# Optimization experiments

Hardware: AMD Instinct MI355X
Metric: run time of the kernel (lower is better)

The kernel has to match this reference:

```python
import jax, jax.numpy as jnp
import numpy as np

D_MODEL = 1024
N_HEADS = 16


def setup_inputs() -> dict:
    key = jax.random.key(0)
    ks = jax.random.split(key, 16)
    B, L, S, D = 4, 2048, 2048, D_MODEL
    inp = {
        "q": jax.random.normal(ks[0], (B, L, D), jnp.float32),
        "k": jax.random.normal(ks[1], (B, S, D), jnp.float32),
        "v": jax.random.normal(ks[2], (B, S, D), jnp.float32),
        "tau": jax.random.uniform(ks[3], (B, 1), jnp.float32, 0.5, 1.5),
        "delta": jax.random.normal(ks[4], (B, S), jnp.float32),
    }
    s = 1.0 / np.sqrt(D)
    inp["Wq"] = jax.random.normal(ks[5], (D, D), jnp.float32) * s
    inp["bq"] = jnp.zeros((D,), jnp.float32)
    inp["Wk"] = jax.random.normal(ks[6], (D, D), jnp.float32) * s
    inp["bk"] = jnp.zeros((D,), jnp.float32)
    inp["Wv"] = jax.random.normal(ks[7], (D, D), jnp.float32) * s
    inp["bv"] = jnp.zeros((D,), jnp.float32)
    inp["Wo"] = jax.random.normal(ks[8], (D, D), jnp.float32) * s
    inp["bo"] = jnp.zeros((D,), jnp.float32)
    return inp


def reference(q, k, v, tau, delta, Wq, bq, Wk, bk, Wv, bv, Wo, bo):
    B, L, D = q.shape
    S = k.shape[1]
    H = N_HEADS
    E = D // H
    # Linear projections (torch Linear: x @ W.T + b), split heads
    qh = (q @ Wq.T + bq).reshape(B, L, H, E)
    kh = (k @ Wk.T + bk).reshape(B, S, H, E)
    vh = (v @ Wv.T + bv).reshape(B, S, H, E)
    scale = 1.0 / np.sqrt(E).astype(np.float32)
    # de-stationary attention: scores * tau + delta, then scaled softmax
    scores = jnp.einsum('blhe,bshe->bhls', qh, kh)
    scores = scores * tau[:, None, None, :] + delta[:, None, None, :]
    a = jax.nn.softmax(scale * scores, axis=-1)  # dropout: eval mode (identity)
    out = jnp.einsum('bhls,bshd->blhd', a, vh).reshape(B, L, D)
    return out @ Wo.T + bo
```

## Files before the change

### kernel.cpp

```cpp
#include <hip/hip_runtime.h>
#include <hip/hip_bf16.h>
#include <stdint.h>

typedef unsigned short u16;
typedef __attribute__((ext_vector_type(8))) short short8;
typedef __attribute__((ext_vector_type(4))) short short4v;
typedef __attribute__((ext_vector_type(4))) float f32x4;
typedef __attribute__((ext_vector_type(16))) float f32x16;
typedef __attribute__((ext_vector_type(2))) unsigned int uint2v;
typedef __attribute__((ext_vector_type(4))) unsigned int uint4v;

#define DEV static __device__ __forceinline__

DEV u16 f2bf(float f) {
  union { float f; unsigned u; } x; x.f = f;
  unsigned r = x.u + 0x7FFFu + ((x.u >> 16) & 1u);
  return (u16)(r >> 16);
}

DEV unsigned cvtpk_bf16(float a, float b) {
  unsigned r;
  asm("v_cvt_pk_bf16_f32 %0, %1, %2" : "=v"(r) : "v"(a), "v"(b));
  return r;
}

DEV void pl32swap(unsigned& a, unsigned& b) {
  asm("v_permlane32_swap_b32 %0, %1" : "+v"(a), "+v"(b));
}

DEV void gld_lds16(const void* g, void* l) {
  __builtin_amdgcn_global_load_lds(
      (const __attribute__((address_space(1))) unsigned int*)(g),
      (__attribute__((address_space(3))) unsigned int*)(l),
      16, 0, 0);
}

DEV f32x16 zero16() {
  f32x16 z = {0.f,0.f,0.f,0.f,0.f,0.f,0.f,0.f,0.f,0.f,0.f,0.f,0.f,0.f,0.f,0.f};
  return z;
}

__global__ void cvt3(const float* __restrict__ a, const float* __restrict__ b,
                     const float* __restrict__ c, u16* __restrict__ oa,
                     u16* __restrict__ ob, u16* __restrict__ oc, int n4) {
  int i = blockIdx.x * blockDim.x + threadIdx.x;
  if (i >= n4) return;
  const float* in = (blockIdx.y == 0) ? a : (blockIdx.y == 1) ? b : c;
  u16* out = (blockIdx.y == 0) ? oa : (blockIdx.y == 1) ? ob : oc;
  float4 v = ((const float4*)in)[i];
  short4v o;
  o[0] = (short)f2bf(v.x); o[1] = (short)f2bf(v.y);
  o[2] = (short)f2bf(v.z); o[3] = (short)f2bf(v.w);
  ((short4v*)out)[i] = o;
}

__global__ void cvt4(const float* __restrict__ a, const float* __restrict__ b,
                     const float* __restrict__ c, const float* __restrict__ d,
                     u16* __restrict__ oa, u16* __restrict__ ob,
                     u16* __restrict__ oc, u16* __restrict__ od, int n4) {
  int i = blockIdx.x * blockDim.x + threadIdx.x;
  if (i >= n4) return;
  const float* in = (blockIdx.y == 0) ? a : (blockIdx.y == 1) ? b : (blockIdx.y == 2) ? c : d;
  u16* out = (blockIdx.y == 0) ? oa : (blockIdx.y == 1) ? ob : (blockIdx.y == 2) ? oc : od;
  float4 v = ((const float4*)in)[i];
  short4v o;
  o[0] = (short)f2bf(v.x); o[1] = (short)f2bf(v.y);
  o[2] = (short)f2bf(v.z); o[3] = (short)f2bf(v.w);
  ((short4v*)out)[i] = o;
}

__global__ void scale_delta(const float* __restrict__ in, float* __restrict__ out, int n4) {
  int i = blockIdx.x * blockDim.x + threadIdx.x;
  if (i >= n4) return;
  constexpr float C = 0.125f * 1.44269504f;
  float4 v = ((const float4*)in)[i];
  f32x4 o = {v.x * C, v.y * C, v.z * C, v.w * C};
  ((f32x4*)out)[i] = o;
}

template<int OMODE>
__global__ __launch_bounds__(256, 2)
void gemm_nt(const u16* __restrict__ A, const u16* __restrict__ Bt,
             const float* __restrict__ bias, void* __restrict__ out) {
  constexpr int Mn = 8192, Nn = 1024, Kn = 1024;
  constexpr int BM = 128, BN = 128, BK = 64;
  __shared__ __align__(16) u16 As[BM * BK];
  __shared__ __align__(16) u16 Bs[BN * BK];
  constexpr int nbn = Nn / BN;
  constexpr int nwg = (Mn / BM) * nbn;
  int bid = blockIdx.x;
  int swz = (bid & 7) * (nwg >> 3) + (bid >> 3);
  int bm = (swz / nbn) * BM;
  int bn = (swz % nbn) * BN;
  int tid = threadIdx.x;
  int lane = tid & 63, w = tid >> 6;
  int l15 = lane & 15, l4 = lane >> 4;
  int wm = (w >> 1) * 64, wn = (w & 1) * 64;
  int swl = (w << 6);

  f32x4 acc[4][4];
#pragma unroll
  for (int i = 0; i < 4; ++i)
#pragma unroll
    for (int j = 0; j < 4; ++j) acc[i][j] = (f32x4){0.f, 0.f, 0.f, 0.f};

  const u16* Ag = A + (size_t)bm * Kn;
  const u16* Bg = Bt + (size_t)bn * Kn;

  for (int kt = 0; kt < Kn / BK; ++kt) {
    int k0 = kt * BK;
#pragma unroll
    for (int j = 0; j < 4; ++j) {
      int flat = j * 256 + tid;
      int row = flat >> 3, u = flat & 7;
      int gu = u ^ (row & 7);
      gld_lds16(Ag + (size_t)row * Kn + k0 + gu * 8, &As[(j * 256 + swl) * 8]);
    }
#pragma unroll
    for (int j = 0; j < 4; ++j) {
      int flat = j * 256 + tid;
      int row = flat >> 3, u = flat & 7;
      int gu = u ^ (row & 7);
      gld_lds16(Bg + (size_t)row * Kn + k0 + gu * 8, &Bs[(j * 256 + swl) * 8]);
    }
    __syncthreads();
#pragma unroll
    for (int ks = 0; ks < 2; ++ks) {
      short8 af[4], bfr[4];
#pragma unroll
      for (int i = 0; i < 4; ++i) {
        int ra = wm + i * 16 + l15;
        int ua = (ks * 4 + l4) ^ (ra & 7);
        af[i] = *(const short8*)&As[ra * 64 + ua * 8];
        int rb = wn + i * 16 + l15;
        int ub = (ks * 4 + l4) ^ (rb & 7);
        bfr[i] = *(const short8*)&Bs[rb * 64 + ub * 8];
      }
#pragma unroll
      for (int mi = 0; mi < 4; ++mi)
#pragma unroll
        for (int ni = 0; ni < 4; ++ni)
          acc[mi][ni] = __builtin_amdgcn_mfma_f32_16x16x32_bf16(af[mi], bfr[ni], acc[mi][ni], 0, 0, 0);
    }
    __syncthreads();
  }

#pragma unroll
  for (int ni = 0; ni < 4; ++ni) {
    int n = bn + wn + ni * 16 + l15;
    float bv = bias[n];
    int h = n >> 6, e = n & 63;
#pragma unroll
    for (int mi = 0; mi < 4; ++mi) {
      int m0 = bm + wm + mi * 16 + l4 * 4;
      if (OMODE == 2) {
        float* o = (float*)out;
#pragma unroll
        for (int j = 0; j < 4; ++j)
          o[(size_t)(m0 + j) * Nn + n] = acc[mi][ni][j] + bv;
      } else if (OMODE == 0) {
        u16* o = (u16*)out;
#pragma unroll
        for (int j = 0; j < 4; ++j) {
          int m = m0 + j;
          int b = m >> 11, l = m & 2047;
          int idx = ((b * 16 + h) * 2048 + l) * 64 + e;
          o[idx] = f2bf(acc[mi][ni][j] + bv);
        }
      } else {
        u16* o = (u16*)out;
        int b = m0 >> 11, s = m0 & 2047;
        short4v pk;
#pragma unroll
        for (int j = 0; j < 4; ++j) pk[j] = (short)f2bf(acc[mi][ni][j] + bv);
        int idx = ((b * 16 + h) * 64 + e) * 2048 + s;
        *(short4v*)&o[idx] = pk;
      }
    }
  }
}

DEV float softpack(const f32x16 sc, float st2, const float* dlp, int hi,
                   short8& f0, short8& f1) {
  float pe[16];
#pragma unroll
  for (int g = 0; g < 4; ++g) {
    f32x4 dlv = *(const f32x4*)(dlp + g * 8 + hi * 4);
#pragma unroll
    for (int m = 0; m < 4; ++m)
      pe[g * 4 + m] = __builtin_amdgcn_exp2f(sc[g * 4 + m] * st2 + dlv[m]);
  }
  float ps = 0.f;
#pragma unroll
  for (int i = 0; i < 16; i += 4) ps += (pe[i] + pe[i + 1]) + (pe[i + 2] + pe[i + 3]);
  unsigned a0 = cvtpk_bf16(pe[0], pe[1]), a1 = cvtpk_bf16(pe[2], pe[3]);
  unsigned b0 = cvtpk_bf16(pe[4], pe[5]), b1 = cvtpk_bf16(pe[6], pe[7]);
  pl32swap(a0, b0);
  pl32swap(a1, b1);
  f0 = __builtin_bit_cast(short8, (uint4v){a0, a1, b0, b1});
  unsigned c0 = cvtpk_bf16(pe[8], pe[9]), c1 = cvtpk_bf16(pe[10], pe[11]);
  unsigned d0 = cvtpk_bf16(pe[12], pe[13]), d1 = cvtpk_bf16(pe[14], pe[15]);
  pl32swap(c0, d0);
  pl32swap(c1, d1);
  f1 = __builtin_bit_cast(short8, (uint4v){c0, c1, d0, d1});
  return ps;
}

__global__ __launch_bounds__(512, 4)
void flash_attn(const u16* __restrict__ qh, const u16* __restrict__ kh,
                const u16* __restrict__ vt, const float* __restrict__ tau,
                const float* __restrict__ dl2g, u16* __restrict__ attn) {
  constexpr int S = 2048, E = 64;
  __shared__ __align__(16) u16 Ks[2][64 * 64];
  __shared__ __align__(16) u16 Vs[2][64 * 64];
  __shared__ __align__(16) float dls[2][64];

  int bh = blockIdx.x & 63, qb = blockIdx.x >> 6;
  int b = bh >> 4, h = bh & 15;
  int tid = threadIdx.x, lane = tid & 63, w = tid >> 6;
  int l31 = lane & 31, hi = lane >> 5;
  int q0 = qb * 256 + w * 32;

  int srow = tid >> 3, sgu = (tid & 7) ^ ((tid >> 3) & 7);

  const u16* Qg = qh + ((size_t)bh * S + q0) * E;
  short8 qf[4];
#pragma unroll
  for (int ec = 0; ec < 4; ++ec)
    qf[ec] = *(const short8*)&Qg[l31 * E + ec * 16 + hi * 8];

  float st2 = tau[b] * (0.125f * 1.44269504f);
  float l_run = 0.f;
  f32x16 oa0 = zero16(), oa1 = zero16();

  const u16* Kg = kh + (size_t)bh * S * E;
  const u16* Vg = vt + (size_t)bh * E * S;
  const float* Dg = dl2g + (size_t)b * S;

  gld_lds16(Kg + (size_t)srow * E + sgu * 8, &Ks[0][w * 512]);
  gld_lds16(Vg + (size_t)srow * S + sgu * 8, &Vs[0][w * 512]);
  if (tid < 16) gld_lds16(Dg + tid * 4, &dls[0][0]);
  __syncthreads();

  for (int t = 0; t < S / 64; ++t) {
    int cur = t & 1, nxt = cur ^ 1;
    if (t < S / 64 - 1) {
      int s1 = (t + 1) * 64;
      gld_lds16(Kg + (size_t)(s1 + srow) * E + sgu * 8, &Ks[nxt][w * 512]);
      gld_lds16(Vg + (size_t)srow * S + s1 + sgu * 8, &Vs[nxt][w * 512]);
      if (tid < 16) gld_lds16(Dg + s1 + tid * 4, &dls[nxt][0]);
    }

    const char* KsB = (const char*)&Ks[cur][0];
    f32x16 sc0 = zero16(), sc1 = zero16();
    __builtin_amdgcn_s_setprio(1);
#pragma unroll
    for (int ec = 0; ec < 4; ++ec) {
      int uo = (((ec * 2 + hi) ^ (l31 & 7)) * 16) + l31 * 128;
      short8 kf0 = *(const short8*)(KsB + uo);
      short8 kf1 = *(const short8*)(KsB + 4096 + uo);
      sc0 = __builtin_amdgcn_mfma_f32_32x32x16_bf16(kf0, qf[ec], sc0, 0, 0, 0);
      sc1 = __builtin_amdgcn_mfma_f32_32x32x16_bf16(kf1, qf[ec], sc1, 0, 0, 0);
    }
    __builtin_amdgcn_s_setprio(0);

    short8 pf0, pf1, pf2, pf3;
    float psum = softpack(sc0, st2, &dls[cur][0], hi, pf0, pf1);
    psum += softpack(sc1, st2, &dls[cur][32], hi, pf2, pf3);
    psum += __shfl_xor(psum, 32);
    l_run += psum;

    const char* VsB = (const char*)&Vs[cur][0];
    __builtin_amdgcn_s_setprio(1);
#pragma unroll
    for (int ksb = 0; ksb < 4; ++ksb) {
      int uo = (((ksb * 2 + hi) ^ (l31 & 7)) * 16) + l31 * 128;
      short8 v0 = *(const short8*)(VsB + uo);
      short8 v1 = *(const short8*)(VsB + 4096 + uo);
      short8 pf = (ksb == 0) ? pf0 : (ksb == 1) ? pf1 : (ksb == 2) ? pf2 : pf3;
      oa0 = __builtin_amdgcn_mfma_f32_32x32x16_bf16(v0, pf, oa0, 0, 0, 0);
      oa1 = __builtin_amdgcn_mfma_f32_32x32x16_bf16(v1, pf, oa1, 0, 0, 0);
    }
    __builtin_amdgcn_s_setprio(0);
    __syncthreads();
  }

  float li = 1.f / l_run;
  u16* Og = attn + ((((size_t)b * 2048 + q0 + l31) * 16 + h) * 64);
#pragma unroll
  for (int g = 0; g < 4; ++g) {
    uint2v s0, s1;
    s0[0] = cvtpk_bf16(oa0[g * 4 + 0] * li, oa0[g * 4 + 1] * li);
    s0[1] = cvtpk_bf16(oa0[g * 4 + 2] * li, oa0[g * 4 + 3] * li);
    *(uint2v*)&Og[g * 8 + hi * 4] = s0;
    s1[0] = cvtpk_bf16(oa1[g * 4 + 0] * li, oa1[g * 4 + 1] * li);
    s1[1] = cvtpk_bf16(oa1[g * 4 + 2] * li, oa1[g * 4 + 3] * li);
    *(uint2v*)&Og[32 + g * 8 + hi * 4] = s1;
  }
}

extern "C" void kernel_launch(void* const* d_in, const int* in_sizes, int n_in,
                              void* d_out, int out_size, void* d_ws, size_t ws_size,
                              hipStream_t stream) {
  const float* q = (const float*)d_in[0];
  const float* k = (const float*)d_in[1];
  const float* v = (const float*)d_in[2];
  const float* tau = (const float*)d_in[3];
  const float* delta = (const float*)d_in[4];
  const float* Wq = (const float*)d_in[5];
  const float* bq = (const float*)d_in[6];
  const float* Wk = (const float*)d_in[7];
  const float* bk = (const float*)d_in[8];
  const float* Wv = (const float*)d_in[9];
  const float* bv = (const float*)d_in[10];
  const float* Wo = (const float*)d_in[11];
  const float* bo = (const float*)d_in[12];

  const size_t SZ_ACT = (size_t)8192 * 1024 * 2;
  const size_t SZ_W = (size_t)1024 * 1024 * 2;
  char* p = (char*)d_ws;
  u16* qbf = (u16*)p; p += SZ_ACT;
  u16* kbf = (u16*)p; p += SZ_ACT;
  u16* vbf = (u16*)p; p += SZ_ACT;
  u16* wq = (u16*)p; p += SZ_W;
  u16* wk = (u16*)p; p += SZ_W;
  u16* wv = (u16*)p; p += SZ_W;
  u16* wo = (u16*)p; p += SZ_W;
  float* dl2g = (float*)p; p += 8192 * 4;
  u16* qhb = (u16*)p; p += SZ_ACT;
  u16* khb = (u16*)p; p += SZ_ACT;
  u16* vtb = (u16*)p; p += SZ_ACT;
  u16* attn = qbf;

  cvt3<<<dim3(8192, 3), 256, 0, stream>>>(q, k, v, qbf, kbf, vbf, 2097152);
  cvt4<<<dim3(1024, 4), 256, 0, stream>>>(Wq, Wk, Wv, Wo, wq, wk, wv, wo, 262144);
  scale_delta<<<8, 256, 0, stream>>>(delta, dl2g, 2048);

  gemm_nt<0><<<512, 256, 0, stream>>>(qbf, wq, bq, qhb);
  gemm_nt<0><<<512, 256, 0, stream>>>(kbf, wk, bk, khb);
  gemm_nt<1><<<512, 256, 0, stream>>>(vbf, wv, bv, vtb);
  flash_attn<<<512, 512, 0, stream>>>(qhb, khb, vtb, tau, dl2g, attn);
  gemm_nt<2><<<512, 256, 0, stream>>>(attn, wo, bo, d_out);
}
```

Baseline: 213.1 us.

## Batch QKV projections into one launch and shrink attention blocks to four waves

The three Q/K/V projection GEMMs become a single 1536-block launch that picks weights, bias and output layout per block, which relies on the contiguous workspace layout of the converted activations and weights. Flash attention now uses 256-thread blocks covering 128 queries, giving 1024 blocks for better occupancy and tail balance. Its K/V LDS staging switches from XOR-swizzled rows to a column-chunk layout with simpler address math. The new LDS layout changes the bank-conflict behaviour, and each block now loads K/V tiles for half as many queries, doubling total K/V traffic.

```diff
diff --git a/kernel.cpp b/kernel.cpp
--- a/kernel.cpp
+++ b/kernel.cpp
@@ -78,16 +78,115 @@
   ((f32x4*)out)[i] = o;
 }
 
-template<int OMODE>
 __global__ __launch_bounds__(256, 2)
-void gemm_nt(const u16* __restrict__ A, const u16* __restrict__ Bt,
-             const float* __restrict__ bias, void* __restrict__ out) {
-  constexpr int Mn = 8192, Nn = 1024, Kn = 1024;
+void gemm_qkv(const u16* __restrict__ A, const u16* __restrict__ W,
+              const float* __restrict__ bq, const float* __restrict__ bk,
+              const float* __restrict__ bv, u16* __restrict__ qhb,
+              u16* __restrict__ khb, u16* __restrict__ vtb) {
+  constexpr int Nn = 1024, Kn = 1024;
   constexpr int BM = 128, BN = 128, BK = 64;
   __shared__ __align__(16) u16 As[BM * BK];
   __shared__ __align__(16) u16 Bs[BN * BK];
   constexpr int nbn = Nn / BN;
-  constexpr int nwg = (Mn / BM) * nbn;
+  constexpr int nwg = (24576 / BM) * nbn;
+  int bid = blockIdx.x;
+  int swz = (bid & 7) * (nwg >> 3) + (bid >> 3);
+  int bm = (swz / nbn) * BM;
+  int bn = (swz % nbn) * BN;
+  int mat = bm >> 13;
+  int bml = bm & 8191;
+  int tid = threadIdx.x;
+  int lane = tid & 63, w = tid >> 6;
+  int l15 = lane & 15, l4 = lane >> 4;
+  int wm = (w >> 1) * 64, wn = (w & 1) * 64;
+  int swl = (w << 6);
+
+  f32x4 acc[4][4];
+#pragma unroll
+  for (int i = 0; i < 4; ++i)
+#pragma unroll
+    for (int j = 0; j < 4; ++j) acc[i][j] = (f32x4){0.f, 0.f, 0.f, 0.f};
+
+  const u16* Ag = A + (size_t)bm * Kn;
+  const u16* Bg = W + ((size_t)mat << 20) + (size_t)bn * Kn;
+
+  for (int kt = 0; kt < Kn / BK; ++kt) {
+    int k0 = kt * BK;
+#pragma unroll
+    for (int j = 0; j < 4; ++j) {
+      int flat = j * 256 + tid;
+      int row = flat >> 3, u = flat & 7;
+      int gu = u ^ (row & 7);
+      gld_lds16(Ag + (size_t)row * Kn + k0 + gu * 8, &As[(j * 256 + swl) * 8]);
+    }
+#pragma unroll
+    for (int j = 0; j < 4; ++j) {
+      int flat = j * 256 + tid;
+      int row = flat >> 3, u = flat & 7;
+      int gu = u ^ (row & 7);
+      gld_lds16(Bg + (size_t)row * Kn + k0 + gu * 8, &Bs[(j * 256 + swl) * 8]);
+    }
+    __syncthreads();
+#pragma unroll
+    for (int ks = 0; ks < 2; ++ks) {
+      short8 af[4], bfr[4];
+#pragma unroll
+      for (int i = 0; i < 4; ++i) {
+        int ra = wm + i * 16 + l15;
+        int ua = (ks * 4 + l4) ^ (ra & 7);
+        af[i] = *(const short8*)&As[ra * 64 + ua * 8];
+        int rb = wn + i * 16 + l15;
+        int ub = (ks * 4 + l4) ^ (rb & 7);
+        bfr[i] = *(const short8*)&Bs[rb * 64 + ub * 8];
+      }
+#pragma unroll
+      for (int mi = 0; mi < 4; ++mi)
+#pragma unroll
+        for (int ni = 0; ni < 4; ++ni)
+          acc[mi][ni] = __builtin_amdgcn_mfma_f32_16x16x32_bf16(af[mi], bfr[ni], acc[mi][ni], 0, 0, 0);
+    }
+    __syncthreads();
+  }
+
+  const float* bias = (mat == 0) ? bq : (mat == 1) ? bk : bv;
+  u16* oQK = (mat == 0) ? qhb : khb;
+#pragma unroll
+  for (int ni = 0; ni < 4; ++ni) {
+    int n = bn + wn + ni * 16 + l15;
+    float bvl = bias[n];
+    int h = n >> 6, e = n & 63;
+#pragma unroll
+    for (int mi = 0; mi < 4; ++mi) {
+      int m0 = bml + wm + mi * 16 + l4 * 4;
+      if (mat < 2) {
+#pragma unroll
+        for (int j = 0; j < 4; ++j) {
+          int m = m0 + j;
+          int b = m >> 11, l = m & 2047;
+          int idx = ((b * 16 + h) * 2048 + l) * 64 + e;
+          oQK[idx] = f2bf(acc[mi][ni][j] + bvl);
+        }
+      } else {
+        int b = m0 >> 11, s = m0 & 2047;
+        short4v pk;
+#pragma unroll
+        for (int j = 0; j < 4; ++j) pk[j] = (short)f2bf(acc[mi][ni][j] + bvl);
+        int idx = ((b * 16 + h) * 64 + e) * 2048 + s;
+        *(short4v*)&vtb[idx] = pk;
+      }
+    }
+  }
+}
+
+__global__ __launch_bounds__(256, 2)
+void gemm_out(const u16* __restrict__ A, const u16* __restrict__ Bt,
+              const float* __restrict__ bias, float* __restrict__ out) {
+  constexpr int Nn = 1024, Kn = 1024;
+  constexpr int BM = 128, BN = 128, BK = 64;
+  __shared__ __align__(16) u16 As[BM * BK];
+  __shared__ __align__(16) u16 Bs[BN * BK];
+  constexpr int nbn = Nn / BN;
+  constexpr int nwg = (8192 / BM) * nbn;
   int bid = blockIdx.x;
   int swz = (bid & 7) * (nwg >> 3) + (bid >> 3);
   int bm = (swz / nbn) * BM;
@@ -148,34 +247,13 @@
 #pragma unroll
   for (int ni = 0; ni < 4; ++ni) {
     int n = bn + wn + ni * 16 + l15;
-    float bv = bias[n];
-    int h = n >> 6, e = n & 63;
+    float bvl = bias[n];
 #pragma unroll
     for (int mi = 0; mi < 4; ++mi) {
       int m0 = bm + wm + mi * 16 + l4 * 4;
-      if (OMODE == 2) {
-        float* o = (float*)out;
-#pragma unroll
-        for (int j = 0; j < 4; ++j)
-          o[(size_t)(m0 + j) * Nn + n] = acc[mi][ni][j] + bv;
-      } else if (OMODE == 0) {
-        u16* o = (u16*)out;
-#pragma unroll
-        for (int j = 0; j < 4; ++j) {
-          int m = m0 + j;
-          int b = m >> 11, l = m & 2047;
-          int idx = ((b * 16 + h) * 2048 + l) * 64 + e;
-          o[idx] = f2bf(acc[mi][ni][j] + bv);
-        }
-      } else {
-        u16* o = (u16*)out;
-        int b = m0 >> 11, s = m0 & 2047;
-        short4v pk;
-#pragma unroll
-        for (int j = 0; j < 4; ++j) pk[j] = (short)f2bf(acc[mi][ni][j] + bv);
-        int idx = ((b * 16 + h) * 64 + e) * 2048 + s;
-        *(short4v*)&o[idx] = pk;
-      }
+#pragma unroll
+      for (int j = 0; j < 4; ++j)
+        out[(size_t)(m0 + j) * Nn + n] = acc[mi][ni][j] + bvl;
     }
   }
 }
@@ -206,22 +284,24 @@
   return ps;
 }
 
-__global__ __launch_bounds__(512, 4)
+__global__ __launch_bounds__(256, 4)
 void flash_attn(const u16* __restrict__ qh, const u16* __restrict__ kh,
                 const u16* __restrict__ vt, const float* __restrict__ tau,
                 const float* __restrict__ dl2g, u16* __restrict__ attn) {
   constexpr int S = 2048, E = 64;
-  __shared__ __align__(16) u16 Ks[2][64 * 64];
-  __shared__ __align__(16) u16 Vs[2][64 * 64];
+  __shared__ __align__(16) u16 Ks[2][4096];
+  __shared__ __align__(16) u16 Vs[2][4096];
   __shared__ __align__(16) float dls[2][64];
 
   int bh = blockIdx.x & 63, qb = blockIdx.x >> 6;
   int b = bh >> 4, h = bh & 15;
   int tid = threadIdx.x, lane = tid & 63, w = tid >> 6;
   int l31 = lane & 31, hi = lane >> 5;
-  int q0 = qb * 256 + w * 32;
-
-  int srow = tid >> 3, sgu = (tid & 7) ^ ((tid >> 3) & 7);
+  int q0 = qb * 128 + w * 32;
+
+  const u16* Kg = kh + (size_t)bh * S * E;
+  const u16* Vg = vt + (size_t)bh * E * S;
+  const float* Dg = dl2g + (size_t)b * S;
 
   const u16* Qg = qh + ((size_t)bh * S + q0) * E;
   short8 qf[4];
@@ -233,21 +313,27 @@
   float l_run = 0.f;
   f32x16 oa0 = zero16(), oa1 = zero16();
 
-  const u16* Kg = kh + (size_t)bh * S * E;
-  const u16* Vg = vt + (size_t)bh * E * S;
-  const float* Dg = dl2g + (size_t)b * S;
-
-  gld_lds16(Kg + (size_t)srow * E + sgu * 8, &Ks[0][w * 512]);
-  gld_lds16(Vg + (size_t)srow * S + sgu * 8, &Vs[0][w * 512]);
+#pragma unroll
+  for (int r = 0; r < 2; ++r) {
+    int c = r * 4 + w;
+    gld_lds16(Kg + (size_t)lane * E + c * 8, &Ks[0][(r * 256 + w * 64) * 8]);
+    gld_lds16(Vg + (size_t)lane * S + c * 8, &Vs[0][(r * 256 + w * 64) * 8]);
+  }
   if (tid < 16) gld_lds16(Dg + tid * 4, &dls[0][0]);
   __syncthreads();
+
+  int kvbase = hi * 1024 + l31 * 16;
 
   for (int t = 0; t < S / 64; ++t) {
     int cur = t & 1, nxt = cur ^ 1;
     if (t < S / 64 - 1) {
       int s1 = (t + 1) * 64;
-      gld_lds16(Kg + (size_t)(s1 + srow) * E + sgu * 8, &Ks[nxt][w * 512]);
-      gld_lds16(Vg + (size_t)srow * S + s1 + sgu * 8, &Vs[nxt][w * 512]);
+#pragma unroll
+      for (int r = 0; r < 2; ++r) {
+        int c = r * 4 + w;
+        gld_lds16(Kg + (size_t)(s1 + lane) * E + c * 8, &Ks[nxt][(r * 256 + w * 64) * 8]);
+        gld_lds16(Vg + (size_t)lane * S + s1 + c * 8, &Vs[nxt][(r * 256 + w * 64) * 8]);
+      }
       if (tid < 16) gld_lds16(Dg + s1 + tid * 4, &dls[nxt][0]);
     }
 
@@ -256,9 +342,8 @@
     __builtin_amdgcn_s_setprio(1);
 #pragma unroll
     for (int ec = 0; ec < 4; ++ec) {
-      int uo = (((ec * 2 + hi) ^ (l31 & 7)) * 16) + l31 * 128;
-      short8 kf0 = *(const short8*)(KsB + uo);
-      short8 kf1 = *(const short8*)(KsB + 4096 + uo);
+      short8 kf0 = *(const short8*)(KsB + kvbase + ec * 2048);
+      short8 kf1 = *(const short8*)(KsB + kvbase + ec * 2048 + 512);
       sc0 = __builtin_amdgcn_mfma_f32_32x32x16_bf16(kf0, qf[ec], sc0, 0, 0, 0);
       sc1 = __builtin_amdgcn_mfma_f32_32x32x16_bf16(kf1, qf[ec], sc1, 0, 0, 0);
     }
@@ -274,9 +359,8 @@
     __builtin_amdgcn_s_setprio(1);
 #pragma unroll
     for (int ksb = 0; ksb < 4; ++ksb) {
-      int uo = (((ksb * 2 + hi) ^ (l31 & 7)) * 16) + l31 * 128;
-      short8 v0 = *(const short8*)(VsB + uo);
-      short8 v1 = *(const short8*)(VsB + 4096 + uo);
+      short8 v0 = *(const short8*)(VsB + kvbase + ksb * 2048);
+      short8 v1 = *(const short8*)(VsB + kvbase + ksb * 2048 + 512);
       short8 pf = (ksb == 0) ? pf0 : (ksb == 1) ? pf1 : (ksb == 2) ? pf2 : pf3;
       oa0 = __builtin_amdgcn_mfma_f32_32x32x16_bf16(v0, pf, oa0, 0, 0, 0);
       oa1 = __builtin_amdgcn_mfma_f32_32x32x16_bf16(v1, pf, oa1, 0, 0, 0);
@@ -336,9 +420,7 @@
   cvt4<<<dim3(1024, 4), 256, 0, stream>>>(Wq, Wk, Wv, Wo, wq, wk, wv, wo, 262144);
   scale_delta<<<8, 256, 0, stream>>>(delta, dl2g, 2048);
 
-  gemm_nt<0><<<512, 256, 0, stream>>>(qbf, wq, bq, qhb);
-  gemm_nt<0><<<512, 256, 0, stream>>>(kbf, wk, bk, khb);
-  gemm_nt<1><<<512, 256, 0, stream>>>(vbf, wv, bv, vtb);
-  flash_attn<<<512, 512, 0, stream>>>(qhb, khb, vtb, tau, dl2g, attn);
-  gemm_nt<2><<<512, 256, 0, stream>>>(attn, wo, bo, d_out);
-}
+  gemm_qkv<<<1536, 256, 0, stream>>>(qbf, wq, bq, bk, bv, qhb, khb, vtb);
+  flash_attn<<<1024, 256, 0, stream>>>(qhb, khb, vtb, tau, dl2g, attn);
+  gemm_out<<<512, 256, 0, stream>>>(attn, wo, bo, (float*)d_out);
+}
```

Result: slower. 220.7 us (+3.5%).
